# Kernel optimization log

Measured on AMD Instinct MI355X. Metric: run time of the kernel, lower is better.

## Reference

```python
import jax, jax.numpy as jnp
import numpy as np

N, E, H = 100000, 1250000, 64
NF, EF = 16, 3
BN_EPS = 1e-5
HALF = H // 2


def setup_inputs() -> dict:
    key = jax.random.key(0)
    ks = jax.random.split(key, 24)
    g = lambda i, shape, s=0.05: jax.random.normal(ks[i], shape, dtype=jnp.float32) * s
    return {
        "x": jax.random.normal(ks[0], (N, NF), dtype=jnp.float32),
        "edge_attr": jax.random.normal(ks[1], (E, EF), dtype=jnp.float32),
        "edge_index": jax.random.randint(ks[2], (2, E), 0, N),
        "W_node": g(3, (NF, H)), "b_node": g(4, (H,)),
        "W_edge": g(5, (EF, H)), "b_edge": g(6, (H,)),
        "W_lin0": g(7, (H, H)), "b_lin0": g(8, (H,)),
        "W_att0": g(9, (2 * H + EF, 1)), "b_att0": g(10, (1,)),
        "W_sage_l": g(11, (H, H)), "b_sage_l": g(12, (H,)),
        "W_sage_r": g(13, (H, H)),
        "W_gcn": g(14, (H, H)), "b_gcn": g(15, (H,)),
        "bn_gamma": jnp.ones((3, H), jnp.float32),
        "bn_beta": jnp.zeros((3, H), jnp.float32),
        "W_r1": g(16, (H, H)), "b_r1": g(17, (H,)),
        "W_r2": g(18, (H, HALF)), "b_r2": g(19, (HALF,)),
        "W_r3": g(20, (HALF, 1)), "b_r3": g(21, (1,)),
    }


def _bn_eval(x, gamma, beta):
    # eval-mode BatchNorm1d with running_mean=0, running_var=1
    return x * (gamma / jnp.sqrt(1.0 + BN_EPS)) + beta


def _edge_att(h, src, dst, edge_attr, W, b, Wa, ba):
    # EdgeAttentionLayer: lin -> per-edge attention MLP -> scatter-add at dst
    h = h @ W + b                                   # [N,H]
    hi, hj = h[dst], h[src]                         # [E,H] gathers
    a = jnp.concatenate([hi, hj, edge_attr], -1) @ Wa + ba   # [E,1]
    a = jax.nn.sigmoid(jax.nn.leaky_relu(a, 0.01))
    return jax.ops.segment_sum(hj * a, dst, num_segments=N)


def _sage(h, src, dst, Wl, bl, Wr):
    # SAGEConv (mean aggregation): lin_l(mean_j x_j) + lin_r(x)
    agg = jax.ops.segment_sum(h[src], dst, num_segments=N)
    cnt = jax.ops.segment_sum(jnp.ones((src.shape[0], 1), h.dtype), dst, num_segments=N)
    mean = agg / jnp.maximum(cnt, 1.0)
    return mean @ Wl + bl + h @ Wr


def _gcn(h, src, dst, W, b):
    # GCNConv with self-loops and symmetric normalization
    hw = h @ W
    loop = jnp.arange(N)
    s = jnp.concatenate([src, loop])
    d = jnp.concatenate([dst, loop])
    deg = jax.ops.segment_sum(jnp.ones(s.shape[0], hw.dtype), d, num_segments=N)
    dis = jnp.where(deg > 0, jax.lax.rsqrt(jnp.maximum(deg, 1.0)), 0.0)
    norm = dis[s] * dis[d]                          # [E+N]
    return jax.ops.segment_sum(hw[s] * norm[:, None], d, num_segments=N) + b


def reference(x, edge_attr, edge_index, W_node, b_node, W_edge, b_edge,
              W_lin0, b_lin0, W_att0, b_att0, W_sage_l, b_sage_l, W_sage_r,
              W_gcn, b_gcn, bn_gamma, bn_beta, W_r1, b_r1, W_r2, b_r2, W_r3, b_r3):
    src, dst = edge_index[0], edge_index[1]
    h = x @ W_node + b_node
    _unused = edge_attr @ W_edge + b_edge  # computed in original forward, never used

    # layer 0: EdgeAttentionLayer + BN + ReLU (+residual; eval dropout = identity)
    ident = h
    h = _edge_att(h, src, dst, edge_attr, W_lin0, b_lin0, W_att0, b_att0)
    h = jax.nn.relu(_bn_eval(h, bn_gamma[0], bn_beta[0])) + ident

    # layer 1: SAGEConv
    ident = h
    h = _sage(h, src, dst, W_sage_l, b_sage_l, W_sage_r)
    h = jax.nn.relu(_bn_eval(h, bn_gamma[1], bn_beta[1])) + ident

    # layer 2: GCNConv
    ident = h
    h = _gcn(h, src, dst, W_gcn, b_gcn)
    h = jax.nn.relu(_bn_eval(h, bn_gamma[2], bn_beta[2])) + ident

    h = jax.nn.relu(h @ W_r1 + b_r1)
    h = jax.nn.relu(h @ W_r2 + b_r2)
    return h @ W_r3 + b_r3  # [N,1]
```

## Files before the change

kernel.cpp:

```cpp
#include <hip/hip_runtime.h>
#include <hip/hip_fp16.h>
#include <math.h>

#define NODES 100000
#define EDGES 1250000
#define HD 64
#define NFD 16
#define CHUNK 1024
#define NCHUNK ((NODES + CHUNK - 1) / CHUNK)
#define BN_INV 0.9999950000374996f
#define LP 65
#define SRCMASK 0x1FFFFu
#define WSCALE (1.0f / 32768.0f)


__global__ void k_hist(const int* __restrict__ ei, int* __restrict__ deg) {
  int e = blockIdx.x * blockDim.x + threadIdx.x;
  if (e < EDGES) atomicAdd(&deg[ei[EDGES + e]], 1);
}

__global__ void k_scan1(const int* __restrict__ deg, int* __restrict__ part) {
  __shared__ int lds[256];
  int t = threadIdx.x, b = blockIdx.x;
  int base = b * CHUNK + t * 4;
  int s = 0;
#pragma unroll
  for (int m = 0; m < 4; m++) { int i = base + m; if (i < NODES) s += deg[i]; }
  lds[t] = s; __syncthreads();
  for (int off = 128; off > 0; off >>= 1) {
    if (t < off) lds[t] += lds[t + off];
    __syncthreads();
  }
  if (t == 0) part[b] = lds[0];
}

__global__ void k_scan2(int* __restrict__ part) {
  if (threadIdx.x == 0 && blockIdx.x == 0) {
    int run = 0;
    for (int c = 0; c < NCHUNK; c++) { int v = part[c]; part[c] = run; run += v; }
  }
}

__global__ void k_scan3(const int* __restrict__ deg, const int* __restrict__ part,
                        int* __restrict__ rowptr, int* __restrict__ cur,
                        float* __restrict__ dis) {
  __shared__ int lds[256];
  int t = threadIdx.x, b = blockIdx.x;
  int base = b * CHUNK + t * 4;
  int dl[4]; int s = 0;
#pragma unroll
  for (int m = 0; m < 4; m++) { int i = base + m; dl[m] = (i < NODES) ? deg[i] : 0; s += dl[m]; }
  lds[t] = s; __syncthreads();
  for (int off = 1; off < 256; off <<= 1) {
    int add = (t >= off) ? lds[t - off] : 0;
    __syncthreads();
    lds[t] += add;
    __syncthreads();
  }
  int run = part[b] + lds[t] - s;
#pragma unroll
  for (int m = 0; m < 4; m++) {
    int i = base + m;
    if (i < NODES) {
      rowptr[i] = run; cur[i] = run;
      dis[i] = 1.0f / sqrtf((float)(dl[m] + 1));
    }
    run += dl[m];
  }
  if (b == 0 && t == 0) rowptr[NODES] = EDGES;
}

__global__ void k_fillatt(const int* __restrict__ ei, const float* __restrict__ ea,
                          const float* __restrict__ cvec, const float* __restrict__ dvec,
                          const float* __restrict__ Wa, const float* __restrict__ ba,
                          int* __restrict__ cur, uint* __restrict__ sa) {
  int e = blockIdx.x * blockDim.x + threadIdx.x;
  if (e >= EDGES) return;
  int s = ei[e], d = ei[EDGES + e];
  float alin = cvec[d] + dvec[s] + ea[3 * e] * Wa[128] + ea[3 * e + 1] * Wa[129] +
               ea[3 * e + 2] * Wa[130] + ba[0];
  float lr = alin >= 0.f ? alin : 0.01f * alin;
  float a = 1.f / (1.f + expf(-lr));
  uint q = min((int)(a * 32768.f + 0.5f), 32767);
  int p = atomicAdd(&cur[d], 1);
  sa[p] = (q << 17) | (uint)s;
}


__device__ __forceinline__ void store16h(__half* dst, const float* v) {
  uint u[8];
#pragma unroll
  for (int j = 0; j < 8; j++) {
    __half2 h = __float22half2_rn(make_float2(v[2 * j], v[2 * j + 1]));
    u[j] = *reinterpret_cast<uint*>(&h);
  }
  uint4* o = (uint4*)dst;
  o[0] = make_uint4(u[0], u[1], u[2], u[3]);
  o[1] = make_uint4(u[4], u[5], u[6], u[7]);
}

__device__ __forceinline__ float4 h4tof4(uint2 u) {
  float2 fa = __half22float2(*reinterpret_cast<__half2*>(&u.x));
  float2 fb = __half22float2(*reinterpret_cast<__half2*>(&u.y));
  return make_float4(fa.x, fa.y, fb.x, fb.y);
}

__device__ __forceinline__ void gstep(const __half* __restrict__ tab,
                                      const uint* __restrict__ sa,
                                      int m, int end, int last, int sub, int col,
                                      bool weighted,
                                      float4& A0, float4& A1, float4& A2, float4& A3) {
  int e0 = m + sub, e1 = e0 + 4, e2 = e0 + 8, e3 = e0 + 12;
  uint s0 = sa[min(e0, last)], s1 = sa[min(e1, last)];
  uint s2 = sa[min(e2, last)], s3 = sa[min(e3, last)];
  float w0 = (e0 < end) ? (weighted ? (float)(s0 >> 17) * WSCALE : 1.f) : 0.f;
  float w1 = (e1 < end) ? (weighted ? (float)(s1 >> 17) * WSCALE : 1.f) : 0.f;
  float w2 = (e2 < end) ? (weighted ? (float)(s2 >> 17) * WSCALE : 1.f) : 0.f;
  float w3 = (e3 < end) ? (weighted ? (float)(s3 >> 17) * WSCALE : 1.f) : 0.f;
  uint2 u0 = *((const uint2*)(tab + (size_t)(s0 & SRCMASK) * HD) + col);
  uint2 u1 = *((const uint2*)(tab + (size_t)(s1 & SRCMASK) * HD) + col);
  uint2 u2 = *((const uint2*)(tab + (size_t)(s2 & SRCMASK) * HD) + col);
  uint2 u3 = *((const uint2*)(tab + (size_t)(s3 & SRCMASK) * HD) + col);
  {
    float4 f = h4tof4(u0);
    A0.x = fmaf(w0, f.x, A0.x); A0.y = fmaf(w0, f.y, A0.y);
    A0.z = fmaf(w0, f.z, A0.z); A0.w = fmaf(w0, f.w, A0.w);
  }
  {
    float4 f = h4tof4(u1);
    A1.x = fmaf(w1, f.x, A1.x); A1.y = fmaf(w1, f.y, A1.y);
    A1.z = fmaf(w1, f.z, A1.z); A1.w = fmaf(w1, f.w, A1.w);
  }
  {
    float4 f = h4tof4(u2);
    A2.x = fmaf(w2, f.x, A2.x); A2.y = fmaf(w2, f.y, A2.y);
    A2.z = fmaf(w2, f.z, A2.z); A2.w = fmaf(w2, f.w, A2.w);
  }
  {
    float4 f = h4tof4(u3);
    A3.x = fmaf(w3, f.x, A3.x); A3.y = fmaf(w3, f.y, A3.y);
    A3.z = fmaf(w3, f.z, A3.z); A3.w = fmaf(w3, f.w, A3.w);
  }
}

__device__ __forceinline__ float4 red4(float4 a0, float4 a1, float4 a2, float4 a3) {
  float4 r;
  r.x = (a0.x + a1.x) + (a2.x + a3.x);
  r.y = (a0.y + a1.y) + (a2.y + a3.y);
  r.z = (a0.z + a1.z) + (a2.z + a3.z);
  r.w = (a0.w + a1.w) + (a2.w + a3.w);
#pragma unroll
  for (int off = 16; off <= 32; off <<= 1) {
    r.x += __shfl_xor(r.x, off); r.y += __shfl_xor(r.y, off);
    r.z += __shfl_xor(r.z, off); r.w += __shfl_xor(r.w, off);
  }
  return r;
}

#define AGG_BODY16(TABLE, WEIGHTED)                                              \
  float4 acc0 = make_float4(0.f, 0.f, 0.f, 0.f);                                 \
  float4 acc1 = make_float4(0.f, 0.f, 0.f, 0.f);                                 \
  float4 acc2 = make_float4(0.f, 0.f, 0.f, 0.f);                                 \
  float4 acc3 = make_float4(0.f, 0.f, 0.f, 0.f);                                 \
  int last = end - 1;                                                            \
  for (int m = start; m < end; m += 16)                                          \
    gstep(TABLE, sa, m, end, last, sub, col, WEIGHTED, acc0, acc1, acc2, acc3);  \
  float4 accr = red4(acc0, acc1, acc2, acc3);


__global__ __launch_bounds__(256) void k_lin0(
    const float* __restrict__ x,
    const float* __restrict__ Wn, const float* __restrict__ bn,
    const float* __restrict__ Wl, const float* __restrict__ bl,
    const float* __restrict__ Wa,
    float* __restrict__ hA, __half* __restrict__ hB16,
    float* __restrict__ cvec, float* __restrict__ dvec) {
  __shared__ float sh[64 * LP];
  __shared__ float sc[4][64], sd[4][64];
  int slot = threadIdx.x & 63;
  int cc = __builtin_amdgcn_readfirstlane(threadIdx.x >> 6);
  int c0 = cc * 16;
  int n0 = blockIdx.x * 64 + slot;
  bool valid = n0 < NODES;
  int n = valid ? n0 : NODES - 1;
  const float4* xr = (const float4*)(x + (size_t)n * NFD);
  float acc[16];
#pragma unroll
  for (int j = 0; j < 16; j++) acc[j] = bn[c0 + j];
#pragma unroll
  for (int q = 0; q < 4; q++) {
    float4 xa = xr[q];
    float xs[4] = {xa.x, xa.y, xa.z, xa.w};
#pragma unroll
    for (int t = 0; t < 4; t++)
#pragma unroll
      for (int j = 0; j < 16; j++)
        acc[j] = fmaf(xs[t], Wn[(q * 4 + t) * HD + c0 + j], acc[j]);
  }
#pragma unroll
  for (int j = 0; j < 16; j++) sh[slot * LP + c0 + j] = acc[j];
  if (valid) {
    float4* o = (float4*)(hA + (size_t)n * HD + c0);
    o[0] = make_float4(acc[0], acc[1], acc[2], acc[3]);
    o[1] = make_float4(acc[4], acc[5], acc[6], acc[7]);
    o[2] = make_float4(acc[8], acc[9], acc[10], acc[11]);
    o[3] = make_float4(acc[12], acc[13], acc[14], acc[15]);
  }
  __syncthreads();
  float a2[16];
#pragma unroll
  for (int j = 0; j < 16; j++) a2[j] = bl[c0 + j];
#pragma unroll 8
  for (int k = 0; k < 64; k++) {
    float hk = sh[slot * LP + k];
#pragma unroll
    for (int j = 0; j < 16; j++)
      a2[j] = fmaf(hk, Wl[k * HD + c0 + j], a2[j]);
  }
  float cn = 0.f, dn = 0.f;
#pragma unroll
  for (int j = 0; j < 16; j++) {
    cn = fmaf(a2[j], Wa[c0 + j], cn);
    dn = fmaf(a2[j], Wa[64 + c0 + j], dn);
  }
  if (valid) store16h(hB16 + (size_t)n * HD + c0, a2);
  sc[cc][slot] = cn;
  sd[cc][slot] = dn;
  __syncthreads();
  if (cc == 0 && valid) {
    cvec[n] = sc[0][slot] + sc[1][slot] + sc[2][slot] + sc[3][slot];
    dvec[n] = sd[0][slot] + sd[1][slot] + sd[2][slot] + sd[3][slot];
  }
}

__global__ __launch_bounds__(256) void k_agg_att(
    const uint* __restrict__ sa, const int* __restrict__ rowptr,
    const float* __restrict__ hA, const __half* __restrict__ hB16,
    const float* __restrict__ g, const float* __restrict__ bt,
    float* __restrict__ hC, __half* __restrict__ hC16) {
  int lane = threadIdx.x & 63;
  int node = __builtin_amdgcn_readfirstlane(blockIdx.x * 4 + (threadIdx.x >> 6));
  if (node >= NODES) return;
  int start = rowptr[node], end = rowptr[node + 1];
  int sub = lane >> 4, col = lane & 15;
  float4 gg = ((const float4*)g)[col];
  float4 bb = ((const float4*)bt)[col];
  float4 ha = *((const float4*)(hA + (size_t)node * HD) + col);
  AGG_BODY16(hB16, true)
  if (lane < 16) {
    float4 v;
    v.x = fmaxf(accr.x * (gg.x * BN_INV) + bb.x, 0.f) + ha.x;
    v.y = fmaxf(accr.y * (gg.y * BN_INV) + bb.y, 0.f) + ha.y;
    v.z = fmaxf(accr.z * (gg.z * BN_INV) + bb.z, 0.f) + ha.z;
    v.w = fmaxf(accr.w * (gg.w * BN_INV) + bb.w, 0.f) + ha.w;
    *((float4*)(hC + (size_t)node * HD) + col) = v;
    __half2 p0 = __float22half2_rn(make_float2(v.x, v.y));
    __half2 p1 = __float22half2_rn(make_float2(v.z, v.w));
    uint2 u;
    u.x = *reinterpret_cast<uint*>(&p0);
    u.y = *reinterpret_cast<uint*>(&p1);
    *((uint2*)(hC16 + (size_t)node * HD) + col) = u;
  }
}

__global__ __launch_bounds__(256) void k_agg_mean16(
    const uint* __restrict__ sa, const int* __restrict__ rowptr,
    const __half* __restrict__ hC16, __half* __restrict__ hM16) {
  int lane = threadIdx.x & 63;
  int node = __builtin_amdgcn_readfirstlane(blockIdx.x * 4 + (threadIdx.x >> 6));
  if (node >= NODES) return;
  int start = rowptr[node], end = rowptr[node + 1];
  int sub = lane >> 4, col = lane & 15;
  AGG_BODY16(hC16, false)
  if (lane < 16) {
    float rdeg = 1.f / fmaxf((float)(end - start), 1.f);
    __half2 p0 = __float22half2_rn(make_float2(accr.x * rdeg, accr.y * rdeg));
    __half2 p1 = __float22half2_rn(make_float2(accr.z * rdeg, accr.w * rdeg));
    uint2 u;
    u.x = *reinterpret_cast<uint*>(&p0);
    u.y = *reinterpret_cast<uint*>(&p1);
    *((uint2*)(hM16 + (size_t)node * HD) + col) = u;
  }
}

__global__ __launch_bounds__(256) void k_sagegcn(
    const __half* __restrict__ hM16, const float* __restrict__ hC,
    const float* __restrict__ Wl, const float* __restrict__ bl,
    const float* __restrict__ Wr, const float* __restrict__ Wg,
    const float* __restrict__ g, const float* __restrict__ bt,
    const float* __restrict__ dis,
    float* __restrict__ hA, __half* __restrict__ hD16) {
  __shared__ float sh[64 * LP];
  int slot = threadIdx.x & 63;
  int cc = __builtin_amdgcn_readfirstlane(threadIdx.x >> 6);
  int c0 = cc * 16;
  int n0 = blockIdx.x * 64 + slot;
  bool valid = n0 < NODES;
  int n = valid ? n0 : NODES - 1;
  {
    const uint4* mp = (const uint4*)(hM16 + (size_t)n * HD + c0);
    uint4 m0 = mp[0], m1 = mp[1];
    uint mm[8] = {m0.x, m0.y, m0.z, m0.w, m1.x, m1.y, m1.z, m1.w};
#pragma unroll
    for (int j = 0; j < 8; j++) {
      float2 f = __half22float2(*reinterpret_cast<__half2*>(&mm[j]));
      sh[slot * LP + c0 + 2 * j] = f.x;
      sh[slot * LP + c0 + 2 * j + 1] = f.y;
    }
  }
  __syncthreads();
  const float4* cr = (const float4*)(hC + (size_t)n * HD);
  float acc[16];
#pragma unroll
  for (int j = 0; j < 16; j++) acc[j] = bl[c0 + j];
#pragma unroll 8
  for (int k = 0; k < 64; k++) {
    float mk = sh[slot * LP + k];
#pragma unroll
    for (int j = 0; j < 16; j++)
      acc[j] = fmaf(mk, Wl[k * HD + c0 + j], acc[j]);
  }
#pragma unroll 4
  for (int q = 0; q < 16; q++) {
    float4 ac = cr[q];
    float cs[4] = {ac.x, ac.y, ac.z, ac.w};
#pragma unroll
    for (int t = 0; t < 4; t++)
#pragma unroll
      for (int j = 0; j < 16; j++)
        acc[j] = fmaf(cs[t], Wr[(q * 4 + t) * HD + c0 + j], acc[j]);
  }
  float tv[16];
  {
    float4 r0 = cr[cc * 4 + 0], r1 = cr[cc * 4 + 1], r2 = cr[cc * 4 + 2], r3 = cr[cc * 4 + 3];
    float rv[16] = {r0.x, r0.y, r0.z, r0.w, r1.x, r1.y, r1.z, r1.w,
                    r2.x, r2.y, r2.z, r2.w, r3.x, r3.y, r3.z, r3.w};
#pragma unroll
    for (int j = 0; j < 16; j++)
      tv[j] = fmaxf(acc[j] * (g[c0 + j] * BN_INV) + bt[c0 + j], 0.f) + rv[j];
  }
  __syncthreads();
#pragma unroll
  for (int j = 0; j < 16; j++) sh[slot * LP + c0 + j] = tv[j];
  if (valid) {
    float4* o = (float4*)(hA + (size_t)n * HD + c0);
    o[0] = make_float4(tv[0], tv[1], tv[2], tv[3]);
    o[1] = make_float4(tv[4], tv[5], tv[6], tv[7]);
    o[2] = make_float4(tv[8], tv[9], tv[10], tv[11]);
    o[3] = make_float4(tv[12], tv[13], tv[14], tv[15]);
  }
  __syncthreads();
  float di = dis[n];
  float a2[16];
#pragma unroll
  for (int j = 0; j < 16; j++) a2[j] = 0.f;
#pragma unroll 8
  for (int k = 0; k < 64; k++) {
    float tk = sh[slot * LP + k];
#pragma unroll
    for (int j = 0; j < 16; j++)
      a2[j] = fmaf(tk, Wg[k * HD + c0 + j], a2[j]);
  }
#pragma unroll
  for (int j = 0; j < 16; j++) a2[j] *= di;
  if (valid) store16h(hD16 + (size_t)n * HD + c0, a2);
}

__global__ __launch_bounds__(256) void k_gcnreg(
    const uint* __restrict__ sa, const int* __restrict__ rowptr,
    const float* __restrict__ dis,
    const float* __restrict__ hA,
    const __half* __restrict__ hD16,
    const float* __restrict__ bg,
    const float* __restrict__ g, const float* __restrict__ bt,
    const float* __restrict__ W1, const float* __restrict__ b1,
    const float* __restrict__ W2, const float* __restrict__ b2,
    const float* __restrict__ W3, const float* __restrict__ b3,
    float* __restrict__ out) {
  __shared__ float sh[64 * LP];
  __shared__ float sred[4][64];
  int lane = threadIdx.x & 63;
  int wu = __builtin_amdgcn_readfirstlane(threadIdx.x >> 6);
  int sub = lane >> 4, col = lane & 15;
  int nbase = blockIdx.x * 64;
  float4 gg = ((const float4*)g)[col];
  float4 bb = ((const float4*)bt)[col];
  float4 bgv = ((const float4*)bg)[col];
  for (int i = 0; i < 16; i++) {
    int slot = wu * 16 + i;
    int nn = min(nbase + slot, NODES - 1);
    int start = rowptr[nn], end = rowptr[nn + 1];
    float di = dis[nn];
    float4 sv = h4tof4(*((const uint2*)(hD16 + (size_t)nn * HD) + col));
    float4 ha = *((const float4*)(hA + (size_t)nn * HD) + col);
    AGG_BODY16(hD16, false)
    if (lane < 16) {
      sh[slot * LP + col * 4 + 0] =
          fmaxf((di * (accr.x + sv.x) + bgv.x) * (gg.x * BN_INV) + bb.x, 0.f) + ha.x;
      sh[slot * LP + col * 4 + 1] =
          fmaxf((di * (accr.y + sv.y) + bgv.y) * (gg.y * BN_INV) + bb.y, 0.f) + ha.y;
      sh[slot * LP + col * 4 + 2] =
          fmaxf((di * (accr.z + sv.z) + bgv.z) * (gg.z * BN_INV) + bb.z, 0.f) + ha.z;
      sh[slot * LP + col * 4 + 3] =
          fmaxf((di * (accr.w + sv.w) + bgv.w) * (gg.w * BN_INV) + bb.w, 0.f) + ha.w;
    }
  }
  __syncthreads();
  int c0 = wu * 16;
  int n0 = nbase + lane;
  bool valid = n0 < NODES;
  int n = valid ? n0 : NODES - 1;
  float acc[16];
#pragma unroll
  for (int j = 0; j < 16; j++) acc[j] = b1[c0 + j];
#pragma unroll 8
  for (int k = 0; k < 64; k++) {
    float rk = sh[lane * LP + k];
#pragma unroll
    for (int j = 0; j < 16; j++)
      acc[j] = fmaf(rk, W1[k * HD + c0 + j], acc[j]);
  }
  float t1v[16];
#pragma unroll
  for (int j = 0; j < 16; j++) t1v[j] = fmaxf(acc[j], 0.f);
  __syncthreads();
#pragma unroll
  for (int j = 0; j < 16; j++) sh[lane * LP + c0 + j] = t1v[j];
  __syncthreads();
  int d0 = wu * 8;
  float a2[8];
#pragma unroll
  for (int j = 0; j < 8; j++) a2[j] = b2[d0 + j];
#pragma unroll 8
  for (int k = 0; k < 64; k++) {
    float tk = sh[lane * LP + k];
#pragma unroll
    for (int j = 0; j < 8; j++)
      a2[j] = fmaf(tk, W2[k * 32 + d0 + j], a2[j]);
  }
  float part = 0.f;
#pragma unroll
  for (int j = 0; j < 8; j++) part = fmaf(fmaxf(a2[j], 0.f), W3[d0 + j], part);
  sred[wu][lane] = part;
  __syncthreads();
  if (wu == 0 && valid)
    out[n] = sred[0][lane] + sred[1][lane] + sred[2][lane] + sred[3][lane] + b3[0];
}


extern "C" void kernel_launch(void* const* d_in, const int* in_sizes, int n_in,
                              void* d_out, int out_size, void* d_ws, size_t ws_size,
                              hipStream_t stream) {
  const float* x      = (const float*)d_in[0];
  const float* ea     = (const float*)d_in[1];
  const int*   ei     = (const int*)d_in[2];
  const float* W_node = (const float*)d_in[3];
  const float* b_node = (const float*)d_in[4];
  const float* W_lin0 = (const float*)d_in[7];
  const float* b_lin0 = (const float*)d_in[8];
  const float* W_att0 = (const float*)d_in[9];
  const float* b_att0 = (const float*)d_in[10];
  const float* W_sl   = (const float*)d_in[11];
  const float* b_sl   = (const float*)d_in[12];
  const float* W_sr   = (const float*)d_in[13];
  const float* W_gcn  = (const float*)d_in[14];
  const float* b_gcn  = (const float*)d_in[15];
  const float* bn_g   = (const float*)d_in[16];
  const float* bn_b   = (const float*)d_in[17];
  const float* W_r1   = (const float*)d_in[18];
  const float* b_r1   = (const float*)d_in[19];
  const float* W_r2   = (const float*)d_in[20];
  const float* b_r2   = (const float*)d_in[21];
  const float* W_r3   = (const float*)d_in[22];
  const float* b_r3   = (const float*)d_in[23];
  float* out = (float*)d_out;

  char* ws = (char*)d_ws;
  size_t o = 0;
  auto alloc = [&](size_t bytes) -> void* {
    void* p = ws + o;
    o += (bytes + 255) & ~(size_t)255;
    return p;
  };
  int*    deg    = (int*)alloc(NODES * 4);
  int*    rowptr = (int*)alloc((NODES + 1) * 4);
  int*    cur    = (int*)alloc(NODES * 4);
  int*    part   = (int*)alloc(256 * 4);
  uint*   sa     = (uint*)alloc((size_t)EDGES * 4);
  float*  hA     = (float*)alloc((size_t)NODES * HD * 4);
  float*  hC     = (float*)alloc((size_t)NODES * HD * 4);
  __half* hB16   = (__half*)alloc((size_t)NODES * HD * 2);
  __half* hC16   = (__half*)alloc((size_t)NODES * HD * 2);
  __half* hD16   = (__half*)alloc((size_t)NODES * HD * 2);
  float*  cvec   = (float*)alloc(NODES * 4);
  float*  dvec   = (float*)alloc(NODES * 4);
  float*  dis    = (float*)alloc(NODES * 4);
  (void)ws_size; (void)in_sizes; (void)n_in; (void)out_size;

  const int EB  = (EDGES + 255) / 256;
  const int NT  = (NODES + 63) / 64;
  const int NBW = (NODES + 3) / 4;

  hipMemsetAsync(deg, 0, NODES * 4, stream);
  k_hist<<<EB, 256, 0, stream>>>(ei, deg);
  k_scan1<<<NCHUNK, 256, 0, stream>>>(deg, part);
  k_scan2<<<1, 64, 0, stream>>>(part);
  k_scan3<<<NCHUNK, 256, 0, stream>>>(deg, part, rowptr, cur, dis);

  k_lin0<<<NT, 256, 0, stream>>>(x, W_node, b_node, W_lin0, b_lin0, W_att0,
                                 hA, hB16, cvec, dvec);
  k_fillatt<<<EB, 256, 0, stream>>>(ei, ea, cvec, dvec, W_att0, b_att0, cur, sa);
  k_agg_att<<<NBW, 256, 0, stream>>>(sa, rowptr, hA, hB16,
                                     bn_g + 0 * HD, bn_b + 0 * HD, hC, hC16);
  k_agg_mean16<<<NBW, 256, 0, stream>>>(sa, rowptr, hC16, hB16);
  k_sagegcn<<<NT, 256, 0, stream>>>(hB16, hC, W_sl, b_sl, W_sr, W_gcn,
                                    bn_g + 1 * HD, bn_b + 1 * HD, dis, hA, hD16);
  k_gcnreg<<<NT, 256, 0, stream>>>(sa, rowptr, dis, hA, hD16, b_gcn,
                                   bn_g + 2 * HD, bn_b + 2 * HD,
                                   W_r1, b_r1, W_r2, b_r2, W_r3, b_r3, out);
}
```

Measured before the change: 308.9 us.

## Split GCN aggregation and regressor MLP into separate kernels

The fused GCN-aggregate-plus-regressor kernel is split in two. A per-node aggregation kernel with one wavefront per node and 25000 blocks writes the post-BN residual features to an fp16 buffer, and a separate MLP kernel reads that buffer back into shared memory. The goal is more parallelism and better latency hiding for the irregular gather, which previously ran serially over 16 nodes per wavefront. The cost is an extra launch, an extra fp16 round trip through global memory, and reduced precision on the regressor input.

```diff
diff --git a/kernel.cpp b/kernel.cpp
--- a/kernel.cpp
+++ b/kernel.cpp
@@ -366,56 +366,73 @@
   if (valid) store16h(hD16 + (size_t)n * HD + c0, a2);
 }
 
-__global__ __launch_bounds__(256) void k_gcnreg(
+__global__ __launch_bounds__(256) void k_agg_gcn16(
     const uint* __restrict__ sa, const int* __restrict__ rowptr,
     const float* __restrict__ dis,
     const float* __restrict__ hA,
     const __half* __restrict__ hD16,
     const float* __restrict__ bg,
     const float* __restrict__ g, const float* __restrict__ bt,
+    __half* __restrict__ hO16) {
+  int lane = threadIdx.x & 63;
+  int node = __builtin_amdgcn_readfirstlane(blockIdx.x * 4 + (threadIdx.x >> 6));
+  if (node >= NODES) return;
+  int start = rowptr[node], end = rowptr[node + 1];
+  int sub = lane >> 4, col = lane & 15;
+  float di = dis[node];
+  float4 sv = h4tof4(*((const uint2*)(hD16 + (size_t)node * HD) + col));
+  float4 ha = *((const float4*)(hA + (size_t)node * HD) + col);
+  float4 gg = ((const float4*)g)[col];
+  float4 bb = ((const float4*)bt)[col];
+  float4 bgv = ((const float4*)bg)[col];
+  AGG_BODY16(hD16, false)
+  if (lane < 16) {
+    float4 v;
+    v.x = fmaxf((di * (accr.x + sv.x) + bgv.x) * (gg.x * BN_INV) + bb.x, 0.f) + ha.x;
+    v.y = fmaxf((di * (accr.y + sv.y) + bgv.y) * (gg.y * BN_INV) + bb.y, 0.f) + ha.y;
+    v.z = fmaxf((di * (accr.z + sv.z) + bgv.z) * (gg.z * BN_INV) + bb.z, 0.f) + ha.z;
+    v.w = fmaxf((di * (accr.w + sv.w) + bgv.w) * (gg.w * BN_INV) + bb.w, 0.f) + ha.w;
+    __half2 p0 = __float22half2_rn(make_float2(v.x, v.y));
+    __half2 p1 = __float22half2_rn(make_float2(v.z, v.w));
+    uint2 u;
+    u.x = *reinterpret_cast<uint*>(&p0);
+    u.y = *reinterpret_cast<uint*>(&p1);
+    *((uint2*)(hO16 + (size_t)node * HD) + col) = u;
+  }
+}
+
+__global__ __launch_bounds__(256) void k_reg(
+    const __half* __restrict__ hO16,
     const float* __restrict__ W1, const float* __restrict__ b1,
     const float* __restrict__ W2, const float* __restrict__ b2,
     const float* __restrict__ W3, const float* __restrict__ b3,
     float* __restrict__ out) {
   __shared__ float sh[64 * LP];
   __shared__ float sred[4][64];
-  int lane = threadIdx.x & 63;
-  int wu = __builtin_amdgcn_readfirstlane(threadIdx.x >> 6);
-  int sub = lane >> 4, col = lane & 15;
-  int nbase = blockIdx.x * 64;
-  float4 gg = ((const float4*)g)[col];
-  float4 bb = ((const float4*)bt)[col];
-  float4 bgv = ((const float4*)bg)[col];
-  for (int i = 0; i < 16; i++) {
-    int slot = wu * 16 + i;
-    int nn = min(nbase + slot, NODES - 1);
-    int start = rowptr[nn], end = rowptr[nn + 1];
-    float di = dis[nn];
-    float4 sv = h4tof4(*((const uint2*)(hD16 + (size_t)nn * HD) + col));
-    float4 ha = *((const float4*)(hA + (size_t)nn * HD) + col);
-    AGG_BODY16(hD16, false)
-    if (lane < 16) {
-      sh[slot * LP + col * 4 + 0] =
-          fmaxf((di * (accr.x + sv.x) + bgv.x) * (gg.x * BN_INV) + bb.x, 0.f) + ha.x;
-      sh[slot * LP + col * 4 + 1] =
-          fmaxf((di * (accr.y + sv.y) + bgv.y) * (gg.y * BN_INV) + bb.y, 0.f) + ha.y;
-      sh[slot * LP + col * 4 + 2] =
-          fmaxf((di * (accr.z + sv.z) + bgv.z) * (gg.z * BN_INV) + bb.z, 0.f) + ha.z;
-      sh[slot * LP + col * 4 + 3] =
-          fmaxf((di * (accr.w + sv.w) + bgv.w) * (gg.w * BN_INV) + bb.w, 0.f) + ha.w;
-    }
-  }
-  __syncthreads();
-  int c0 = wu * 16;
-  int n0 = nbase + lane;
+  int slot = threadIdx.x & 63;
+  int cc = __builtin_amdgcn_readfirstlane(threadIdx.x >> 6);
+  int c0 = cc * 16;
+  int n0 = blockIdx.x * 64 + slot;
   bool valid = n0 < NODES;
   int n = valid ? n0 : NODES - 1;
+  {
+    const uint4* mp = (const uint4*)(hO16 + (size_t)n * HD + c0);
+    uint4 m0 = mp[0], m1 = mp[1];
+    uint mm[8] = {m0.x, m0.y, m0.z, m0.w, m1.x, m1.y, m1.z, m1.w};
+#pragma unroll
+    for (int j = 0; j < 8; j++) {
+      float2 f = __half22float2(*reinterpret_cast<__half2*>(&mm[j]));
+      sh[slot * LP + c0 + 2 * j] = f.x;
+      sh[slot * LP + c0 + 2 * j + 1] = f.y;
+    }
+  }
+  __syncthreads();
   float acc[16];
 #pragma unroll
   for (int j = 0; j < 16; j++) acc[j] = b1[c0 + j];
 #pragma unroll 8
   for (int k = 0; k < 64; k++) {
-    float rk = sh[lane * LP + k];
+    float rk = sh[slot * LP + k];
 #pragma unroll
     for (int j = 0; j < 16; j++)
       acc[j] = fmaf(rk, W1[k * HD + c0 + j], acc[j]);
@@ -425,15 +442,15 @@
   for (int j = 0; j < 16; j++) t1v[j] = fmaxf(acc[j], 0.f);
   __syncthreads();
 #pragma unroll
-  for (int j = 0; j < 16; j++) sh[lane * LP + c0 + j] = t1v[j];
-  __syncthreads();
-  int d0 = wu * 8;
+  for (int j = 0; j < 16; j++) sh[slot * LP + c0 + j] = t1v[j];
+  __syncthreads();
+  int d0 = cc * 8;
   float a2[8];
 #pragma unroll
   for (int j = 0; j < 8; j++) a2[j] = b2[d0 + j];
 #pragma unroll 8
   for (int k = 0; k < 64; k++) {
-    float tk = sh[lane * LP + k];
+    float tk = sh[slot * LP + k];
 #pragma unroll
     for (int j = 0; j < 8; j++)
       a2[j] = fmaf(tk, W2[k * 32 + d0 + j], a2[j]);
@@ -441,10 +458,10 @@
   float part = 0.f;
 #pragma unroll
   for (int j = 0; j < 8; j++) part = fmaf(fmaxf(a2[j], 0.f), W3[d0 + j], part);
-  sred[wu][lane] = part;
-  __syncthreads();
-  if (wu == 0 && valid)
-    out[n] = sred[0][lane] + sred[1][lane] + sred[2][lane] + sred[3][lane] + b3[0];
+  sred[cc][slot] = part;
+  __syncthreads();
+  if (cc == 0 && valid)
+    out[n] = sred[0][slot] + sred[1][slot] + sred[2][slot] + sred[3][slot] + b3[0];
 }
 
 
@@ -515,7 +532,7 @@
   k_agg_mean16<<<NBW, 256, 0, stream>>>(sa, rowptr, hC16, hB16);
   k_sagegcn<<<NT, 256, 0, stream>>>(hB16, hC, W_sl, b_sl, W_sr, W_gcn,
                                     bn_g + 1 * HD, bn_b + 1 * HD, dis, hA, hD16);
-  k_gcnreg<<<NT, 256, 0, stream>>>(sa, rowptr, dis, hA, hD16, b_gcn,
-                                   bn_g + 2 * HD, bn_b + 2 * HD,
-                                   W_r1, b_r1, W_r2, b_r2, W_r3, b_r3, out);
-}
+  k_agg_gcn16<<<NBW, 256, 0, stream>>>(sa, rowptr, dis, hA, hD16, b_gcn,
+                                       bn_g + 2 * HD, bn_b + 2 * HD, hC16);
+  k_reg<<<NT, 256, 0, stream>>>(hC16, W_r1, b_r1, W_r2, b_r2, W_r3, b_r3, out);
+}
```

Measured after the change: 305.2 us. About the same (-1.2%).
